# Performance work log

Measured on AMD Instinct MI355X. Metric: run time of the kernel, lower is better.

The kernel has to match this reference:

```python
import jax, jax.numpy as jnp
import numpy as np

EPS = 1e-6


def _safe_norm(x, axis, keepdims=True):
    # sqrt with zero-safe gradient (double-where trick)
    sq = (x * x).sum(axis=axis, keepdims=keepdims)
    safe = jnp.where(sq > 0, sq, 1.0)
    return jnp.where(sq > 0, jnp.sqrt(safe), 0.0)


def _complex_coord_norm(lig, pro, lig_mask, pro_mask, set_weights):
    # 'length' norm over the joint complex: scale each set so the mean vector
    # length over all real (lig + pro) nodes is ~1, with a learnable per-set weight.
    lig_len = _safe_norm(lig, axis=-1, keepdims=False) * lig_mask   # [B,S,Nl]
    pro_len = _safe_norm(pro, axis=-1, keepdims=False) * pro_mask   # [B,S,Np]
    total_len = lig_len.sum(-1) + pro_len.sum(-1)                   # [B,S]
    n_atoms = lig_mask.sum(-1) + pro_mask.sum(-1)                   # [B,S]
    mean_len = (total_len / n_atoms)[..., None, None]               # [B,S,1,1]
    w = set_weights[None, :, None, None]
    lig = lig * w / (mean_len + EPS) * lig_mask[..., None]
    pro = pro * w / (mean_len + EPS) * pro_mask[..., None]
    return lig, pro


def setup_inputs() -> dict:
    key = jax.random.key(0)
    ks = jax.random.split(key, 8)
    B, S, P, Nl, Np = 8, 64, 64, 128, 256
    scale = 1.0 / np.sqrt(S)
    return {
        "lig_coord_sets": jax.random.normal(ks[0], (B, S, Nl, 3), jnp.float32),
        "messages": jax.random.normal(ks[1], (B, Nl, Nl + Np, P), jnp.float32),
        "adj_matrix": jax.random.randint(ks[2], (B, Nl, Nl + Np), 0, 2, jnp.int32),
        "lig_node_mask": jnp.ones((B, S, Nl), jnp.float32),
        "pro_coord_sets": jax.random.normal(ks[3], (B, S, Np, 3), jnp.float32),
        "pro_node_mask": jnp.ones((B, S, Np), jnp.float32),
        "lig_proj_w": jax.random.normal(ks[4], (P, S), jnp.float32) * scale,
        "pro_proj_w": jax.random.normal(ks[5], (P, S), jnp.float32) * scale,
        "attn_proj_w": jax.random.normal(ks[6], (S, P), jnp.float32) * scale,
        "set_weights": jnp.ones((S,), jnp.float32),
    }


def reference(lig_coord_sets, messages, adj_matrix, lig_node_mask,
              pro_coord_sets, pro_node_mask,
              lig_proj_w, pro_proj_w, attn_proj_w, set_weights):
    B, S, Nl, _ = lig_coord_sets.shape
    lig, pro = _complex_coord_norm(lig_coord_sets, pro_coord_sets,
                                   lig_node_mask, pro_node_mask, set_weights)
    # Linear over the sets dim: [B,S,N,3] -> [B,3,N,P]
    lig_p = jnp.einsum('bsnc,ps->bcnp', lig, lig_proj_w)
    pro_p = jnp.einsum('bsnc,ps->bcnp', pro, pro_proj_w)
    proj = jnp.concatenate([lig_p, pro_p], axis=2)        # [B,3,N,P]
    # pairwise vector diffs, ligand queries only (matches post-hoc slice in torch)
    vec = proj[:, :, :Nl, None, :] - proj[:, :, None, :, :]   # [B,3,Nl,N,P]
    lengths = _safe_norm(vec, axis=1)                          # [B,1,Nl,N,P]
    norm_dists = vec / (lengths + EPS)
    attn_mask = jnp.where(adj_matrix > 0, 0.0, -jnp.inf)       # [B,Nl,N]
    attn = jax.nn.softmax(messages + attn_mask[..., None], axis=2)  # [B,Nl,N,P]
    upd = jnp.einsum('bcinp,binp->bcip', norm_dists, attn)     # [B,3,Nl,P]
    weights = jnp.sqrt((attn * attn).sum(axis=2))              # [B,Nl,P]
    upd = upd * weights[:, None]
    # attn_proj (P -> S) + transpose(1,-1): [B,3,Nl,P] -> [B,S,Nl,3]
    return jnp.einsum('bcip,sp->bsic', upd, attn_proj_w)
```

## Files before the change

kernel.cpp:

```cpp
#include <hip/hip_runtime.h>
#include <hip/hip_bf16.h>
#include <math.h>

#define B   8
#define S   64
#define NL  128
#define NPRO 256
#define NN  384
#define P   64
#define NGRP 8
#define EPSF 1e-6f

__global__ __launch_bounds__(64) void meanlen_kernel(
    const float* __restrict__ lig, const float* __restrict__ ligmask,
    const float* __restrict__ pro, const float* __restrict__ promask,
    float* __restrict__ meanlen)
{
    int blk = blockIdx.x;
    int t = threadIdx.x;
    float suml = 0.f, cnt = 0.f;

    const float* lbase = lig + (size_t)blk * NL * 3;
    const float* lm    = ligmask + (size_t)blk * NL;
    for (int n = t; n < NL; n += 64) {
        float x = lbase[n*3+0], y = lbase[n*3+1], z = lbase[n*3+2];
        float mk = lm[n];
        suml += sqrtf(x*x + y*y + z*z) * mk;
        cnt  += mk;
    }
    const float* pbase = pro + (size_t)blk * NPRO * 3;
    const float* pm    = promask + (size_t)blk * NPRO;
    for (int n = t; n < NPRO; n += 64) {
        float x = pbase[n*3+0], y = pbase[n*3+1], z = pbase[n*3+2];
        float mk = pm[n];
        suml += sqrtf(x*x + y*y + z*z) * mk;
        cnt  += mk;
    }
    for (int off = 32; off > 0; off >>= 1) {
        suml += __shfl_down(suml, off);
        cnt  += __shfl_down(cnt,  off);
    }
    if (t == 0) meanlen[blk] = suml / cnt;
}

__global__ __launch_bounds__(64) void proj_kernel(
    const float* __restrict__ lig, const float* __restrict__ pro,
    const float* __restrict__ ligmask, const float* __restrict__ promask,
    const float* __restrict__ ligw, const float* __restrict__ prow,
    const float* __restrict__ sw, const float* __restrict__ meanlen,
    float* __restrict__ projx, float* __restrict__ projy, float* __restrict__ projz)
{
    int blk = blockIdx.x;
    int b = blk / (NN / NGRP);
    int g = blk - b * (NN / NGRP);
    int nbase = g * NGRP;
    int t = threadIdx.x;
    bool isl = (nbase < NL);

    __shared__ float wl[64][65];
    const float* w = isl ? ligw : prow;
    for (int row = 0; row < 64; ++row) wl[row][t] = w[row * 64 + t];

    __shared__ float cs[NGRP][3][64];
    {
        int s = t;
        float gfac = sw[s] / (meanlen[b * S + s] + EPSF);
        for (int nn = 0; nn < NGRP; ++nn) {
            int n = nbase + nn;
            float mk, X, Y, Z;
            if (isl) {
                size_t base = ((size_t)b * S + s) * NL + n;
                mk = ligmask[base];
                X = lig[base*3+0]; Y = lig[base*3+1]; Z = lig[base*3+2];
            } else {
                size_t base = ((size_t)b * S + s) * NPRO + (n - NL);
                mk = promask[base];
                X = pro[base*3+0]; Y = pro[base*3+1]; Z = pro[base*3+2];
            }
            float gg = gfac * mk;
            cs[nn][0][s] = X * gg;
            cs[nn][1][s] = Y * gg;
            cs[nn][2][s] = Z * gg;
        }
    }
    __syncthreads();

    for (int nn = 0; nn < NGRP; ++nn) {
        float a0 = 0.f, a1 = 0.f, a2 = 0.f;
        #pragma unroll 8
        for (int s = 0; s < 64; ++s) {
            float wv = wl[t][s];
            a0 += cs[nn][0][s] * wv;
            a1 += cs[nn][1][s] * wv;
            a2 += cs[nn][2][s] * wv;
        }
        size_t base = ((size_t)b * NN + nbase + nn) * P;
        projx[base + t] = a0;
        projy[base + t] = a1;
        projz[base + t] = a2;
    }
}

__global__ __launch_bounds__(256) void partial_kernel(
    const float* __restrict__ messages,
    const int*   __restrict__ adj,
    const float* __restrict__ projx,
    const float* __restrict__ projy,
    const float* __restrict__ projz,
    float* __restrict__ partial)
{
    int blk = blockIdx.x;
    int b  = blk >> 6;
    int nh = (blk >> 3) & 7;
    int ic = blk & 7;
    int t = threadIdx.x;
    int wave = t >> 6;
    int p = t & 63;
    int n0 = nh * 48 + wave * 12;

    __shared__ float amk[16][48];
    __shared__ float wavepart[2][4][5][64];

    for (int idx = t; idx < 16 * 48; idx += 256) {
        int il = idx / 48, q = idx - il * 48;
        amk[il][q] = adj[((size_t)b * NL + ic * 16 + il) * NN + nh * 48 + q] > 0
                     ? 0.f : -INFINITY;
    }

    float xnx[12], xny[12], xnz[12];
    size_t pbase = ((size_t)b * NN + n0) * 64 + p;
    #pragma unroll
    for (int k = 0; k < 12; ++k) {
        xnx[k] = projx[pbase + (size_t)k * 64];
        xny[k] = projy[pbase + (size_t)k * 64];
        xnz[k] = projz[pbase + (size_t)k * 64];
    }
    __syncthreads();

    #pragma unroll 1
    for (int il = 0; il < 16; ++il) {
        size_t row = (size_t)b * NL + ic * 16 + il;
        size_t xidx = ((size_t)b * NN + ic * 16 + il) * 64 + p;
        float xix = projx[xidx], xiy = projy[xidx], xiz = projz[xidx];

        const float* mb = messages + (row * NN + n0) * 64 + p;
        float m[12];
        #pragma unroll
        for (int k = 0; k < 12; ++k) m[k] = mb[(size_t)k * 64];

        float s1 = 0.f, s2 = 0.f, a0 = 0.f, a1 = 0.f, a2 = 0.f;
        #pragma unroll
        for (int k = 0; k < 12; ++k) {
            float am = amk[il][wave * 12 + k];
            float d0 = xix - xnx[k], d1 = xiy - xny[k], d2 = xiz - xnz[k];
            float sq = fmaf(d0, d0, fmaf(d1, d1, d2 * d2));
            float inv; asm("v_rsq_f32 %0, %1" : "=v"(inv) : "v"(sq));
            inv = fminf(inv, 1e30f);
            float xe = fmaf(m[k], 1.44269504f, am);
            float e; asm("v_exp_f32 %0, %1" : "=v"(e) : "v"(xe));
            float ei = e * inv;
            s1 += e; s2 = fmaf(e, e, s2);
            a0 = fmaf(ei, d0, a0); a1 = fmaf(ei, d1, a1); a2 = fmaf(ei, d2, a2);
        }

        int buf = il & 1;
        wavepart[buf][wave][0][p] = s1;
        wavepart[buf][wave][1][p] = s2;
        wavepart[buf][wave][2][p] = a0;
        wavepart[buf][wave][3][p] = a1;
        wavepart[buf][wave][4][p] = a2;
        __syncthreads();

        for (int idx = t; idx < 320; idx += 256) {
            int acc = idx >> 6, pp = idx & 63;
            float v = wavepart[buf][0][acc][pp] + wavepart[buf][1][acc][pp]
                    + wavepart[buf][2][acc][pp] + wavepart[buf][3][acc][pp];
            partial[((row * 8 + nh) * 5 + acc) * 64 + pp] = v;
        }
    }
}

__global__ __launch_bounds__(192) void combine_kernel(
    const float* __restrict__ partial,
    const float* __restrict__ attn_w,
    float* __restrict__ out)
{
    int blk = blockIdx.x;
    int b = blk >> 7;
    int i = blk & (NL - 1);
    int t = threadIdx.x;

    __shared__ float upd[3][64];

    if (t < 64) {
        float s1 = 0.f, s2 = 0.f, a0 = 0.f, a1 = 0.f, a2 = 0.f;
        #pragma unroll
        for (int nh = 0; nh < 8; ++nh) {
            size_t base = (((size_t)blk * 8 + nh) * 5) * 64 + t;
            s1 += partial[base];
            s2 += partial[base + 64];
            a0 += partial[base + 128];
            a1 += partial[base + 192];
            a2 += partial[base + 256];
        }
        float wgt = sqrtf(s2) / (s1 * s1);
        upd[0][t] = a0 * wgt;
        upd[1][t] = a1 * wgt;
        upd[2][t] = a2 * wgt;
    }
    __syncthreads();

    int s = t & 63, c = t >> 6;
    const float4* aw4 = (const float4*)attn_w + (size_t)s * 16;
    float o = 0.f;
    #pragma unroll
    for (int q = 0; q < 16; ++q) {
        float4 w4 = aw4[q];
        o = fmaf(upd[c][q*4+0], w4.x, o);
        o = fmaf(upd[c][q*4+1], w4.y, o);
        o = fmaf(upd[c][q*4+2], w4.z, o);
        o = fmaf(upd[c][q*4+3], w4.w, o);
    }
    out[(((size_t)b * S + s) * NL + i) * 3 + c] = o;
}

extern "C" void kernel_launch(void* const* d_in, const int* in_sizes, int n_in,
                              void* d_out, int out_size, void* d_ws, size_t ws_size,
                              hipStream_t stream)
{
    const float* lig      = (const float*)d_in[0];
    const float* messages = (const float*)d_in[1];
    const int*   adj      = (const int*)  d_in[2];
    const float* ligmask  = (const float*)d_in[3];
    const float* pro      = (const float*)d_in[4];
    const float* promask  = (const float*)d_in[5];
    const float* ligw     = (const float*)d_in[6];
    const float* prow     = (const float*)d_in[7];
    const float* attnw    = (const float*)d_in[8];
    const float* sw       = (const float*)d_in[9];
    float* out = (float*)d_out;

    const size_t plane = (size_t)B * NN * P;
    float* meanlen = (float*)d_ws;
    float* projx   = (float*)((char*)d_ws + 2048);
    float* projy   = projx + plane;
    float* projz   = projy + plane;
    float* partial = (float*)((char*)d_ws + (4u << 20));

    meanlen_kernel<<<B * S, 64, 0, stream>>>(lig, ligmask, pro, promask, meanlen);
    proj_kernel<<<B * (NN / NGRP), 64, 0, stream>>>(lig, pro, ligmask, promask,
                                                    ligw, prow, sw, meanlen,
                                                    projx, projy, projz);
    partial_kernel<<<B * 8 * 8, 256, 0, stream>>>(messages, adj,
                                                  projx, projy, projz, partial);
    combine_kernel<<<B * NL, 192, 0, stream>>>(partial, attnw, out);
}
```

Baseline: 59.86 us.

## Repartition partial kernel into more blocks and drop intra-block wave reduction

Result: faster. 57.39 us (-4.1%).

```diff
diff --git a/kernel.cpp b/kernel.cpp
--- a/kernel.cpp
+++ b/kernel.cpp
@@ -101,7 +101,7 @@
     }
 }
 
-__global__ __launch_bounds__(256) void partial_kernel(
+__global__ __launch_bounds__(256, 4) void partial_kernel(
     const float* __restrict__ messages,
     const int*   __restrict__ adj,
     const float* __restrict__ projx,
@@ -110,27 +110,28 @@
     float* __restrict__ partial)
 {
     int blk = blockIdx.x;
-    int b  = blk >> 6;
-    int nh = (blk >> 3) & 7;
-    int ic = blk & 7;
+    int b  = blk >> 7;
+    int g  = (blk >> 5) & 3;
+    int ic = blk & 31;
     int t = threadIdx.x;
     int wave = t >> 6;
     int p = t & 63;
-    int n0 = nh * 48 + wave * 12;
-
-    __shared__ float amk[16][48];
-    __shared__ float wavepart[2][4][5][64];
-
-    for (int idx = t; idx < 16 * 48; idx += 256) {
-        int il = idx / 48, q = idx - il * 48;
-        amk[il][q] = adj[((size_t)b * NL + ic * 16 + il) * NN + nh * 48 + q] > 0
+    int nsl = g * 4 + wave;
+    int n0 = nsl * 24;
+    int i0 = ic * 4;
+
+    __shared__ float amk[4][96];
+
+    for (int idx = t; idx < 4 * 96; idx += 256) {
+        int il = idx / 96, q = idx - il * 96;
+        amk[il][q] = adj[((size_t)b * NL + i0 + il) * NN + g * 96 + q] > 0
                      ? 0.f : -INFINITY;
     }
 
-    float xnx[12], xny[12], xnz[12];
+    float xnx[24], xny[24], xnz[24];
     size_t pbase = ((size_t)b * NN + n0) * 64 + p;
     #pragma unroll
-    for (int k = 0; k < 12; ++k) {
+    for (int k = 0; k < 24; ++k) {
         xnx[k] = projx[pbase + (size_t)k * 64];
         xny[k] = projy[pbase + (size_t)k * 64];
         xnz[k] = projz[pbase + (size_t)k * 64];
@@ -138,45 +139,43 @@
     __syncthreads();
 
     #pragma unroll 1
-    for (int il = 0; il < 16; ++il) {
-        size_t row = (size_t)b * NL + ic * 16 + il;
-        size_t xidx = ((size_t)b * NN + ic * 16 + il) * 64 + p;
+    for (int il = 0; il < 4; ++il) {
+        int i = i0 + il;
+        size_t row = (size_t)b * NL + i;
+        size_t xidx = ((size_t)b * NN + i) * 64 + p;
         float xix = projx[xidx], xiy = projy[xidx], xiz = projz[xidx];
 
         const float* mb = messages + (row * NN + n0) * 64 + p;
-        float m[12];
+        float s1 = 0.f, s2 = 0.f, a0 = 0.f, a1 = 0.f, a2 = 0.f;
+
         #pragma unroll
-        for (int k = 0; k < 12; ++k) m[k] = mb[(size_t)k * 64];
-
-        float s1 = 0.f, s2 = 0.f, a0 = 0.f, a1 = 0.f, a2 = 0.f;
-        #pragma unroll
-        for (int k = 0; k < 12; ++k) {
-            float am = amk[il][wave * 12 + k];
-            float d0 = xix - xnx[k], d1 = xiy - xny[k], d2 = xiz - xnz[k];
-            float sq = fmaf(d0, d0, fmaf(d1, d1, d2 * d2));
-            float inv; asm("v_rsq_f32 %0, %1" : "=v"(inv) : "v"(sq));
-            inv = fminf(inv, 1e30f);
-            float xe = fmaf(m[k], 1.44269504f, am);
-            float e; asm("v_exp_f32 %0, %1" : "=v"(e) : "v"(xe));
-            float ei = e * inv;
-            s1 += e; s2 = fmaf(e, e, s2);
-            a0 = fmaf(ei, d0, a0); a1 = fmaf(ei, d1, a1); a2 = fmaf(ei, d2, a2);
-        }
-
-        int buf = il & 1;
-        wavepart[buf][wave][0][p] = s1;
-        wavepart[buf][wave][1][p] = s2;
-        wavepart[buf][wave][2][p] = a0;
-        wavepart[buf][wave][3][p] = a1;
-        wavepart[buf][wave][4][p] = a2;
-        __syncthreads();
-
-        for (int idx = t; idx < 320; idx += 256) {
-            int acc = idx >> 6, pp = idx & 63;
-            float v = wavepart[buf][0][acc][pp] + wavepart[buf][1][acc][pp]
-                    + wavepart[buf][2][acc][pp] + wavepart[buf][3][acc][pp];
-            partial[((row * 8 + nh) * 5 + acc) * 64 + pp] = v;
-        }
+        for (int hb = 0; hb < 2; ++hb) {
+            float m[12];
+            #pragma unroll
+            for (int k = 0; k < 12; ++k)
+                m[k] = mb[(size_t)(hb * 12 + k) * 64];
+            #pragma unroll
+            for (int k = 0; k < 12; ++k) {
+                int kk = hb * 12 + k;
+                float am = amk[il][wave * 24 + kk];
+                float d0 = xix - xnx[kk], d1 = xiy - xny[kk], d2 = xiz - xnz[kk];
+                float sq = fmaf(d0, d0, fmaf(d1, d1, d2 * d2));
+                float inv; asm("v_rsq_f32 %0, %1" : "=v"(inv) : "v"(sq));
+                inv = fminf(inv, 1e30f);
+                float xe = fmaf(m[k], 1.44269504f, am);
+                float e; asm("v_exp_f32 %0, %1" : "=v"(e) : "v"(xe));
+                float ei = e * inv;
+                s1 += e; s2 = fmaf(e, e, s2);
+                a0 = fmaf(ei, d0, a0); a1 = fmaf(ei, d1, a1); a2 = fmaf(ei, d2, a2);
+            }
+        }
+
+        float* dst = partial + ((row * 16 + nsl) * 5) * 64 + p;
+        dst[0]   = s1;
+        dst[64]  = s2;
+        dst[128] = a0;
+        dst[192] = a1;
+        dst[256] = a2;
     }
 }
 
@@ -195,8 +194,8 @@
     if (t < 64) {
         float s1 = 0.f, s2 = 0.f, a0 = 0.f, a1 = 0.f, a2 = 0.f;
         #pragma unroll
-        for (int nh = 0; nh < 8; ++nh) {
-            size_t base = (((size_t)blk * 8 + nh) * 5) * 64 + t;
+        for (int nh = 0; nh < 16; ++nh) {
+            size_t base = (((size_t)blk * 16 + nh) * 5) * 64 + t;
             s1 += partial[base];
             s2 += partial[base + 64];
             a0 += partial[base + 128];
@@ -251,7 +250,7 @@
     proj_kernel<<<B * (NN / NGRP), 64, 0, stream>>>(lig, pro, ligmask, promask,
                                                     ligw, prow, sw, meanlen,
                                                     projx, projy, projz);
-    partial_kernel<<<B * 8 * 8, 256, 0, stream>>>(messages, adj,
-                                                  projx, projy, projz, partial);
+    partial_kernel<<<B * 4 * 32, 256, 0, stream>>>(messages, adj,
+                                                   projx, projy, projz, partial);
     combine_kernel<<<B * NL, 192, 0, stream>>>(partial, attnw, out);
 }
```
